# Kernel tuning notes

Measured on AMD Instinct MI355X. Metric: run time of the kernel, lower is better.

Reference implementation:

```python
import jax, jax.numpy as jnp
import numpy as np

B, T, C = 8, 2048, 768
HEAD = 64
NUM_REL = 2048


def setup_inputs() -> dict:
    key = jax.random.key(0)
    k1, k2, k3, k4, k5 = jax.random.split(key, 5)
    input_tensor = jax.random.normal(k1, (B, T, C), dtype=jnp.float32)
    # torch Linear(C, HEAD, bias=False): y = x @ W.T, W:[HEAD,C]; store as [C,HEAD]
    Wq = jax.random.normal(k2, (C, HEAD), dtype=jnp.float32) * (C ** -0.5)
    Wk = jax.random.normal(k3, (C, HEAD), dtype=jnp.float32) * (C ** -0.5)
    Wv = jax.random.normal(k4, (C, HEAD), dtype=jnp.float32) * (C ** -0.5)
    bias_table = jax.random.normal(k5, (NUM_REL, 1), dtype=jnp.float32)
    return {"input_tensor": input_tensor, "Wq": Wq, "Wk": Wk, "Wv": Wv, "bias_table": bias_table}


def reference(input_tensor, Wq, Wk, Wv, bias_table):
    Bsz, Tlen, _ = input_tensor.shape
    q = input_tensor @ Wq  # [B,T,H]
    k = input_tensor @ Wk
    v = input_tensor @ Wv
    scale = q.shape[-1] ** -0.5
    scores = jnp.einsum('bqh,bkh->bqk', q, k) * scale  # [B,T,T]
    # relative position bias: clamp(i - j, 0, NUM_REL-1)
    qpos = jnp.arange(Tlen)[:, None]
    kpos = jnp.arange(Tlen)[None, :]
    rel = jnp.clip(qpos - kpos, 0, bias_table.shape[0] - 1)
    bias = bias_table[rel, 0]  # [T,T]
    scores = scores + bias
    causal = kpos <= qpos  # True where allowed
    scores = jnp.where(causal, scores, -jnp.inf)
    attn = jax.nn.softmax(scores, axis=-1)
    return jnp.einsum('bqk,bkh->bqh', attn, v)
```

## Files before the change

kernel.cpp:

```cpp
#include <hip/hip_runtime.h>
#include <hip/hip_bf16.h>

typedef __attribute__((ext_vector_type(8))) short bf16x8;
typedef __attribute__((ext_vector_type(4))) short short4v;
typedef __attribute__((ext_vector_type(4))) float f32x4;

#define B_SZ 8
#define T_SZ 2048
#define C_SZ 768
#define H_SZ 64

__device__ __forceinline__ short f2bs(float f){
  __hip_bfloat16 h = __float2bfloat16(f);
  short s; __builtin_memcpy(&s, &h, 2); return s;
}
__device__ __forceinline__ f32x4 vmax4(f32x4 a, f32x4 b){
  f32x4 r; r[0]=fmaxf(a[0],b[0]); r[1]=fmaxf(a[1],b[1]);
  r[2]=fmaxf(a[2],b[2]); r[3]=fmaxf(a[3],b[3]); return r;
}
__device__ __forceinline__ void gload16(const void* g, void* l){
  __builtin_amdgcn_global_load_lds(
    (const __attribute__((address_space(1))) unsigned int*)g,
    (__attribute__((address_space(3))) unsigned int*)l, 16, 0, 0);
}

__global__ __launch_bounds__(256) void prep_wt(const float* __restrict__ Wq, const float* __restrict__ Wk,
                        const float* __restrict__ Wv, const float* __restrict__ bias,
                        short* __restrict__ Wt, float* __restrict__ bsc){
  int tid = threadIdx.x;
  if (blockIdx.x >= 36){
    int i = (blockIdx.x - 36)*256 + tid;
    bsc[i] = bias[i] * 1.44269504f;
    return;
  }
  __shared__ float tile[64][65];
  int mat = blockIdx.x / 12, kblk = blockIdx.x % 12;
  const float* W = (mat == 0) ? Wq : (mat == 1 ? Wk : Wv);
  int k0 = kblk * 64;
  int r = tid >> 2, cq = (tid & 3) * 16;
  #pragma unroll
  for (int i = 0; i < 4; ++i){
    float4 v = *reinterpret_cast<const float4*>(&W[(k0 + r)*H_SZ + cq + i*4]);
    tile[r][cq + i*4 + 0] = v.x; tile[r][cq + i*4 + 1] = v.y;
    tile[r][cq + i*4 + 2] = v.z; tile[r][cq + i*4 + 3] = v.w;
  }
  __syncthreads();
  int n = tid >> 2, kq = (tid & 3) * 16;
  bf16x8 o0, o1;
  #pragma unroll
  for (int e = 0; e < 8; ++e){
    o0[e] = f2bs(tile[kq + e][n]);
    o1[e] = f2bs(tile[kq + 8 + e][n]);
  }
  *reinterpret_cast<bf16x8*>(&Wt[(mat*64 + n)*C_SZ + k0 + kq])     = o0;
  *reinterpret_cast<bf16x8*>(&Wt[(mat*64 + n)*C_SZ + k0 + kq + 8]) = o1;
}

__global__ __launch_bounds__(512, 2) void qkv_gemm(const float* __restrict__ x, const short* __restrict__ Wt,
                         short* __restrict__ qb, short* __restrict__ kb, short* __restrict__ vT){
  __shared__ float As[2][2048];
  __shared__ short Bs[2][12288];
  int tid = threadIdx.x;
  int wv = tid >> 6, lane = tid & 63, lhi = lane >> 4, llo = lane & 15;
  int wm = wv >> 2, wn = wv & 3;
  long R0 = (long)blockIdx.x * 32;

  int srow = tid >> 4;
  int schunk = (tid & 15) ^ (srow & 7);
  const float* gsrcA = &x[(R0 + srow)*C_SZ + schunk*4];
  float* ldstA = &As[0][wv*256];

  int bn = tid >> 3;
  int bc = (tid & 7) ^ (bn & 7);
  const short* gsrcB0 = &Wt[(  0 + bn)*C_SZ + bc*8];
  const short* gsrcB1 = &Wt[( 64 + bn)*C_SZ + bc*8];
  const short* gsrcB2 = &Wt[(128 + bn)*C_SZ + bc*8];
  short* ldstB = &Bs[0][wv*512];

  f32x4 acc[3];
  #pragma unroll
  for (int j = 0; j < 3; ++j) acc[j] = (f32x4){0.f,0.f,0.f,0.f};

  int rr = wm*16 + llo;
  int r7 = rr & 7, lhi2 = lhi*2;
  int c0 = ((lhi2    ) ^ r7) << 2;
  int c1 = ((lhi2 + 1) ^ r7) << 2;
  int c2 = ((lhi2 + 8) ^ r7) << 2;
  int c3 = ((lhi2 + 9) ^ r7) << 2;
  int nrow[3];
  #pragma unroll
  for (int j = 0; j < 3; ++j) nrow[j] = (wn*48 + j*16 + llo)*64;
  int llo7 = llo & 7;
  int bo0 = ((    lhi) ^ llo7)*8;
  int bo1 = ((4 + lhi) ^ llo7)*8;

#define STAGE(T, BUF) { \
    gload16(gsrcA  + (T)*64, ldstA + (BUF)*2048); \
    gload16(gsrcB0 + (T)*64, ldstB + (BUF)*12288); \
    gload16(gsrcB1 + (T)*64, ldstB + (BUF)*12288 + 4096); \
    gload16(gsrcB2 + (T)*64, ldstB + (BUF)*12288 + 8192); }

  STAGE(0, 0);
  __syncthreads();

  for (int t = 0; t < 12; ++t){
    int cb = t & 1;
    if (t < 11) STAGE(t + 1, cb ^ 1);
    const float* Ar = &As[cb][rr*64];
    f32x4 a0 = *reinterpret_cast<const f32x4*>(Ar + c0);
    f32x4 a1 = *reinterpret_cast<const f32x4*>(Ar + c1);
    f32x4 a2 = *reinterpret_cast<const f32x4*>(Ar + c2);
    f32x4 a3 = *reinterpret_cast<const f32x4*>(Ar + c3);
    bf16x8 af0, af1;
    #pragma unroll
    for (int e = 0; e < 4; ++e){
      af0[e]   = f2bs(a0[e]); af0[4+e] = f2bs(a1[e]);
      af1[e]   = f2bs(a2[e]); af1[4+e] = f2bs(a3[e]);
    }
    const short* Br = &Bs[cb][0];
    #pragma unroll
    for (int j = 0; j < 3; ++j){
      bf16x8 b0 = *reinterpret_cast<const bf16x8*>(Br + nrow[j] + bo0);
      bf16x8 b1 = *reinterpret_cast<const bf16x8*>(Br + nrow[j] + bo1);
      acc[j] = __builtin_amdgcn_mfma_f32_16x16x32_bf16(af0, b0, acc[j], 0, 0, 0);
      acc[j] = __builtin_amdgcn_mfma_f32_16x16x32_bf16(af1, b1, acc[j], 0, 0, 0);
    }
    __syncthreads();
  }
#undef STAGE

  long mbase = R0 + wm*16 + lhi*4;
  #pragma unroll
  for (int j = 0; j < 3; ++j){
    int n = wn*48 + j*16 + llo;
    int mat = n >> 6, c = n & 63;
    if (mat == 2){
      long b = mbase >> 11, t = mbase & 2047;
      short4v p;
      #pragma unroll
      for (int reg = 0; reg < 4; ++reg) p[reg] = f2bs(acc[j][reg]);
      *reinterpret_cast<short4v*>(&vT[(b*H_SZ + c)*T_SZ + t]) = p;
    } else {
      short* dst = (mat == 0) ? qb : kb;
      #pragma unroll
      for (int reg = 0; reg < 4; ++reg)
        dst[(mbase + reg)*H_SZ + c] = f2bs(acc[j][reg]);
    }
  }
}

__global__ __launch_bounds__(512, 4) void attn_fwd(const short* __restrict__ qb, const short* __restrict__ kb,
                        const short* __restrict__ vT, const float* __restrict__ bsc,
                        float* __restrict__ out){
  __shared__ float bias_s[2048];
  __shared__ short P_lds[8][2][1152];
  __shared__ float m_part[8][16];
  __shared__ float l_part[8][4][16];
  float* OP = (float*)&P_lds[0][0][0];

  int tid = threadIdx.x;
  for (int i = tid; i < 2048; i += 512) bias_s[i] = bsc[i];

  int wv = tid >> 6, lane = tid & 63, lhi = lane >> 4, llo = lane & 15;
  int b = blockIdx.x & 7, jj = blockIdx.x >> 3;
  int qtA = jj, qtB = 127 - jj;
  int qA = qtA*16 + llo, qB = qtB*16 + llo;
  int nktA = (qtA >> 2) + 1, nktB = (qtB >> 2) + 1;

  const short* qrA = &qb[((long)(b*T_SZ + qA))*H_SZ + lhi*8];
  const short* qrB = &qb[((long)(b*T_SZ + qB))*H_SZ + lhi*8];
  bf16x8 qfA0 = *reinterpret_cast<const bf16x8*>(qrA);
  bf16x8 qfA1 = *reinterpret_cast<const bf16x8*>(qrA + 32);
  bf16x8 qfB0 = *reinterpret_cast<const bf16x8*>(qrB);
  bf16x8 qfB1 = *reinterpret_cast<const bf16x8*>(qrB + 32);
  const short* kbase = kb + (long)b*T_SZ*H_SZ;
  const short* vbase = vT + (long)b*H_SZ*T_SZ;
  __syncthreads();

  float mA = -1e30f, lA = 0.f, mB = -1e30f, lB = 0.f;
  f32x4 oA[4], oB[4];
  #pragma unroll
  for (int df = 0; df < 4; ++df){ oA[df] = (f32x4){0.f,0.f,0.f,0.f}; oB[df] = (f32x4){0.f,0.f,0.f,0.f}; }

#define SM(S, M, L, O, QV, TI, PB0, PB1) {                                  \
    _Pragma("unroll") for (int f = 0; f < 4; ++f)                           \
      _Pragma("unroll") for (int rg = 0; rg < 4; ++rg){                     \
        int kv = kv0 + f*16 + lhi*4 + rg;                                   \
        int rel = (QV) - kv;                                                \
        float bv = bias_s[rel > 0 ? rel : 0];                               \
        S[f][rg] = (rel >= 0) ? fmaf(S[f][rg], 0.18033688f, bv) : -1e30f; } \
    f32x4 tm = vmax4(vmax4(S[0], S[1]), vmax4(S[2], S[3]));                 \
    float pmax = fmaxf(fmaxf(tm[0], tm[1]), fmaxf(tm[2], tm[3]));           \
    if (!__all(pmax <= M + 8.0f)){                                          \
      float rm = fmaxf(pmax, __shfl_xor(pmax, 16));                         \
      rm = fmaxf(rm, __shfl_xor(rm, 32));                                   \
      float mnew = fmaxf(M, rm);                                            \
      float corr = exp2f(M - mnew);                                         \
      M = mnew; L *= corr;                                                  \
      _Pragma("unroll") for (int df = 0; df < 4; ++df) O[df] = O[df]*corr; }\
    _Pragma("unroll") for (int f = 0; f < 4; ++f){                          \
      short4v pk;                                                           \
      _Pragma("unroll") for (int rg = 0; rg < 4; ++rg){                     \
        float p = exp2f(S[f][rg] - M); S[f][rg] = p; pk[rg] = f2bs(p); }    \
      *reinterpret_cast<short4v*>(&P_lds[wv][TI][llo*72 + f*16 + lhi*4]) = pk; } \
    f32x4 va = (S[0] + S[1]) + (S[2] + S[3]);                               \
    L += (va[0] + va[1]) + (va[2] + va[3]);                                 \
    PB0 = *reinterpret_cast<const bf16x8*>(&P_lds[wv][TI][llo*72 + lhi*8]); \
    PB1 = *reinterpret_cast<const bf16x8*>(&P_lds[wv][TI][llo*72 + 32 + lhi*8]); }

  for (int c = wv; c < nktB; c += 8){
    int kv0 = c * 64;
    bool doA = c < nktA;
    f32x4 sA[4], sB[4];
    #pragma unroll
    for (int f = 0; f < 4; ++f){
      const short* kr = kbase + (long)(kv0 + f*16 + llo)*H_SZ + lhi*8;
      bf16x8 k0 = *reinterpret_cast<const bf16x8*>(kr);
      bf16x8 k1 = *reinterpret_cast<const bf16x8*>(kr + 32);
      f32x4 t = (f32x4){0.f,0.f,0.f,0.f};
      t = __builtin_amdgcn_mfma_f32_16x16x32_bf16(k0, qfB0, t, 0, 0, 0);
      t = __builtin_amdgcn_mfma_f32_16x16x32_bf16(k1, qfB1, t, 0, 0, 0);
      sB[f] = t;
      f32x4 u = (f32x4){0.f,0.f,0.f,0.f};
      u = __builtin_amdgcn_mfma_f32_16x16x32_bf16(k0, qfA0, u, 0, 0, 0);
      u = __builtin_amdgcn_mfma_f32_16x16x32_bf16(k1, qfA1, u, 0, 0, 0);
      sA[f] = u;
    }
    bf16x8 pbB0, pbB1;
    SM(sB, mB, lB, oB, qB, 1, pbB0, pbB1);
    if (doA){
      bf16x8 pbA0, pbA1;
      SM(sA, mA, lA, oA, qA, 0, pbA0, pbA1);
      #pragma unroll
      for (int df = 0; df < 4; ++df){
        const short* vr = vbase + (long)(df*16 + llo)*T_SZ + kv0 + lhi*8;
        bf16x8 v0 = *reinterpret_cast<const bf16x8*>(vr);
        bf16x8 v1 = *reinterpret_cast<const bf16x8*>(vr + 32);
        oB[df] = __builtin_amdgcn_mfma_f32_16x16x32_bf16(v0, pbB0, oB[df], 0, 0, 0);
        oB[df] = __builtin_amdgcn_mfma_f32_16x16x32_bf16(v1, pbB1, oB[df], 0, 0, 0);
        oA[df] = __builtin_amdgcn_mfma_f32_16x16x32_bf16(v0, pbA0, oA[df], 0, 0, 0);
        oA[df] = __builtin_amdgcn_mfma_f32_16x16x32_bf16(v1, pbA1, oA[df], 0, 0, 0);
      }
    } else {
      #pragma unroll
      for (int df = 0; df < 4; ++df){
        const short* vr = vbase + (long)(df*16 + llo)*T_SZ + kv0 + lhi*8;
        bf16x8 v0 = *reinterpret_cast<const bf16x8*>(vr);
        bf16x8 v1 = *reinterpret_cast<const bf16x8*>(vr + 32);
        oB[df] = __builtin_amdgcn_mfma_f32_16x16x32_bf16(v0, pbB0, oB[df], 0, 0, 0);
        oB[df] = __builtin_amdgcn_mfma_f32_16x16x32_bf16(v1, pbB1, oB[df], 0, 0, 0);
      }
    }
  }
#undef SM

#define MERGE(O, M, L, QT) {                                                \
    _Pragma("unroll") for (int df = 0; df < 4; ++df)                        \
      _Pragma("unroll") for (int rg = 0; rg < 4; ++rg)                      \
        OP[wv*1152 + llo*65 + df*16 + lhi*4 + rg] = O[df][rg];              \
    l_part[wv][lhi][llo] = L;                                               \
    if (lhi == 0) m_part[wv][llo] = M;                                      \
    __syncthreads();                                                        \
    { int idx = tid;                                                        \
      _Pragma("unroll") for (int rep = 0; rep < 2; ++rep){                  \
        int row = idx >> 6, d = idx & 63;                                   \
        float mstar = m_part[0][row];                                       \
        _Pragma("unroll") for (int w = 1; w < 8; ++w)                       \
          mstar = fmaxf(mstar, m_part[w][row]);                             \
        float lsum = 0.f, osum = 0.f;                                       \
        _Pragma("unroll") for (int w = 0; w < 8; ++w){                      \
          float sc = exp2f(m_part[w][row] - mstar);                         \
          lsum += sc * (l_part[w][0][row] + l_part[w][1][row]               \
                      + l_part[w][2][row] + l_part[w][3][row]);             \
          osum += sc * OP[w*1152 + row*65 + d]; }                           \
        out[((long)(b*T_SZ + (QT)*16 + row))*H_SZ + d] = osum / lsum;       \
        idx += 512; } }                                                     \
    __syncthreads(); }

  MERGE(oB, mB, lB, qtB);
  MERGE(oA, mA, lA, qtA);
#undef MERGE
}

extern "C" void kernel_launch(void* const* d_in, const int* in_sizes, int n_in,
                              void* d_out, int out_size, void* d_ws, size_t ws_size,
                              hipStream_t stream){
  const float* x    = (const float*)d_in[0];
  const float* Wq   = (const float*)d_in[1];
  const float* Wk   = (const float*)d_in[2];
  const float* Wv   = (const float*)d_in[3];
  const float* bias = (const float*)d_in[4];
  float* out = (float*)d_out;

  const size_t NTOK = (size_t)B_SZ * T_SZ * H_SZ;
  short* qb = (short*)d_ws;
  short* kb = qb + NTOK;
  short* vT = kb + NTOK;
  short* Wt = vT + NTOK;
  float* bsc = (float*)(Wt + 192*C_SZ);

  prep_wt<<<44, 256, 0, stream>>>(Wq, Wk, Wv, bias, Wt, bsc);
  qkv_gemm<<<512, 512, 0, stream>>>(x, Wt, qb, kb, vT);
  attn_fwd<<<512, 512, 0, stream>>>(qb, kb, vT, bsc, out);
}
```

Before: 58.33 us.

## Triple-buffer QKV GEMM with smaller K tiles and raise MFMA wave priority

```diff
diff --git a/kernel.cpp b/kernel.cpp
--- a/kernel.cpp
+++ b/kernel.cpp
@@ -58,74 +58,72 @@
 
 __global__ __launch_bounds__(512, 2) void qkv_gemm(const float* __restrict__ x, const short* __restrict__ Wt,
                          short* __restrict__ qb, short* __restrict__ kb, short* __restrict__ vT){
-  __shared__ float As[2][2048];
-  __shared__ short Bs[2][12288];
+  __shared__ float As[3][1024];
+  __shared__ short Bs[3][6144];
   int tid = threadIdx.x;
   int wv = tid >> 6, lane = tid & 63, lhi = lane >> 4, llo = lane & 15;
   int wm = wv >> 2, wn = wv & 3;
   long R0 = (long)blockIdx.x * 32;
 
-  int srow = tid >> 4;
-  int schunk = (tid & 15) ^ (srow & 7);
-  const float* gsrcA = &x[(R0 + srow)*C_SZ + schunk*4];
-  float* ldstA = &As[0][wv*256];
-
-  int bn = tid >> 3;
-  int bc = (tid & 7) ^ (bn & 7);
-  const short* gsrcB0 = &Wt[(  0 + bn)*C_SZ + bc*8];
-  const short* gsrcB1 = &Wt[( 64 + bn)*C_SZ + bc*8];
-  const short* gsrcB2 = &Wt[(128 + bn)*C_SZ + bc*8];
-  short* ldstB = &Bs[0][wv*512];
+  int r8 = lane >> 3, p8 = lane & 7;
+  int r4 = lane >> 2, p4 = lane & 3;
+  const char* src0; int sstr0; char* dst0; int dstr0;
+  if (wv < 4){
+    src0 = (const char*)&x[(R0 + wv*8 + r8)*C_SZ + ((p8 ^ (r8 & 7)) << 2)];
+    sstr0 = C_SZ ? 128 : 0;
+    sstr0 = 128;
+    dst0 = (char*)&As[0][wv*256]; dstr0 = 4096;
+  } else {
+    src0 = (const char*)&Wt[((wv-4)*16 + r4)*C_SZ + ((p4 ^ (r4 & 3)) << 3)];
+    sstr0 = 64;
+    dst0 = (char*)&Bs[0][(wv-4)*512]; dstr0 = 12288;
+  }
+  const char* src1 = (const char*)&Wt[((4+wv)*16 + r4)*C_SZ + ((p4 ^ (r4 & 3)) << 3)];
+  char* dst1 = (char*)&Bs[0][(4+wv)*512];
+
+#define STAGE(T, BUF) { \
+    gload16(src0 + (T)*sstr0, dst0 + (BUF)*dstr0); \
+    gload16(src1 + (T)*64,    dst1 + (BUF)*12288); }
 
   f32x4 acc[3];
   #pragma unroll
   for (int j = 0; j < 3; ++j) acc[j] = (f32x4){0.f,0.f,0.f,0.f};
 
   int rr = wm*16 + llo;
-  int r7 = rr & 7, lhi2 = lhi*2;
-  int c0 = ((lhi2    ) ^ r7) << 2;
-  int c1 = ((lhi2 + 1) ^ r7) << 2;
-  int c2 = ((lhi2 + 8) ^ r7) << 2;
-  int c3 = ((lhi2 + 9) ^ r7) << 2;
-  int nrow[3];
-  #pragma unroll
-  for (int j = 0; j < 3; ++j) nrow[j] = (wn*48 + j*16 + llo)*64;
-  int llo7 = llo & 7;
-  int bo0 = ((    lhi) ^ llo7)*8;
-  int bo1 = ((4 + lhi) ^ llo7)*8;
-
-#define STAGE(T, BUF) { \
-    gload16(gsrcA  + (T)*64, ldstA + (BUF)*2048); \
-    gload16(gsrcB0 + (T)*64, ldstB + (BUF)*12288); \
-    gload16(gsrcB1 + (T)*64, ldstB + (BUF)*12288 + 4096); \
-    gload16(gsrcB2 + (T)*64, ldstB + (BUF)*12288 + 8192); }
+  int r7 = rr & 7;
+  int c0x = rr*32 + (((2*lhi    ) ^ r7) << 2);
+  int c1x = rr*32 + (((2*lhi + 1) ^ r7) << 2);
+  int nof[3];
+  #pragma unroll
+  for (int j = 0; j < 3; ++j){
+    int n = wn*48 + j*16 + llo;
+    nof[j] = n*32 + ((lhi ^ (n & 3)) << 3);
+  }
 
   STAGE(0, 0);
-  __syncthreads();
-
-  for (int t = 0; t < 12; ++t){
-    int cb = t & 1;
-    if (t < 11) STAGE(t + 1, cb ^ 1);
-    const float* Ar = &As[cb][rr*64];
-    f32x4 a0 = *reinterpret_cast<const f32x4*>(Ar + c0);
-    f32x4 a1 = *reinterpret_cast<const f32x4*>(Ar + c1);
-    f32x4 a2 = *reinterpret_cast<const f32x4*>(Ar + c2);
-    f32x4 a3 = *reinterpret_cast<const f32x4*>(Ar + c3);
-    bf16x8 af0, af1;
+  STAGE(1, 1);
+
+  #pragma unroll
+  for (int t = 0; t < 24; ++t){
+    if (t < 23) asm volatile("s_waitcnt vmcnt(2)" ::: "memory");
+    else        asm volatile("s_waitcnt vmcnt(0)" ::: "memory");
+    __builtin_amdgcn_sched_barrier(0);
+    __builtin_amdgcn_s_barrier();
+    __builtin_amdgcn_sched_barrier(0);
+    if (t < 22) STAGE(t + 2, (t + 2) % 3);
+    int cb = t % 3;
+    const float* Ar = &As[cb][0];
+    f32x4 a0 = *reinterpret_cast<const f32x4*>(Ar + c0x);
+    f32x4 a1 = *reinterpret_cast<const f32x4*>(Ar + c1x);
+    bf16x8 af;
     #pragma unroll
-    for (int e = 0; e < 4; ++e){
-      af0[e]   = f2bs(a0[e]); af0[4+e] = f2bs(a1[e]);
-      af1[e]   = f2bs(a2[e]); af1[4+e] = f2bs(a3[e]);
-    }
+    for (int e = 0; e < 4; ++e){ af[e] = f2bs(a0[e]); af[4+e] = f2bs(a1[e]); }
     const short* Br = &Bs[cb][0];
     #pragma unroll
     for (int j = 0; j < 3; ++j){
-      bf16x8 b0 = *reinterpret_cast<const bf16x8*>(Br + nrow[j] + bo0);
-      bf16x8 b1 = *reinterpret_cast<const bf16x8*>(Br + nrow[j] + bo1);
-      acc[j] = __builtin_amdgcn_mfma_f32_16x16x32_bf16(af0, b0, acc[j], 0, 0, 0);
-      acc[j] = __builtin_amdgcn_mfma_f32_16x16x32_bf16(af1, b1, acc[j], 0, 0, 0);
+      bf16x8 bf = *reinterpret_cast<const bf16x8*>(Br + nof[j]);
+      acc[j] = __builtin_amdgcn_mfma_f32_16x16x32_bf16(af, bf, acc[j], 0, 0, 0);
     }
-    __syncthreads();
   }
 #undef STAGE
 
@@ -212,6 +210,7 @@
     int kv0 = c * 64;
     bool doA = c < nktA;
     f32x4 sA[4], sB[4];
+    __builtin_amdgcn_s_setprio(1);
     #pragma unroll
     for (int f = 0; f < 4; ++f){
       const short* kr = kbase + (long)(kv0 + f*16 + llo)*H_SZ + lhi*8;
@@ -226,11 +225,13 @@
       u = __builtin_amdgcn_mfma_f32_16x16x32_bf16(k1, qfA1, u, 0, 0, 0);
       sA[f] = u;
     }
+    __builtin_amdgcn_s_setprio(0);
     bf16x8 pbB0, pbB1;
     SM(sB, mB, lB, oB, qB, 1, pbB0, pbB1);
     if (doA){
       bf16x8 pbA0, pbA1;
       SM(sA, mA, lA, oA, qA, 0, pbA0, pbA1);
+      __builtin_amdgcn_s_setprio(1);
       #pragma unroll
       for (int df = 0; df < 4; ++df){
         const short* vr = vbase + (long)(df*16 + llo)*T_SZ + kv0 + lhi*8;
@@ -241,7 +242,9 @@
         oA[df] = __builtin_amdgcn_mfma_f32_16x16x32_bf16(v0, pbA0, oA[df], 0, 0, 0);
         oA[df] = __builtin_amdgcn_mfma_f32_16x16x32_bf16(v1, pbA1, oA[df], 0, 0, 0);
       }
+      __builtin_amdgcn_s_setprio(0);
     } else {
+      __builtin_amdgcn_s_setprio(1);
       #pragma unroll
       for (int df = 0; df < 4; ++df){
         const short* vr = vbase + (long)(df*16 + llo)*T_SZ + kv0 + lhi*8;
@@ -250,6 +253,7 @@
         oB[df] = __builtin_amdgcn_mfma_f32_16x16x32_bf16(v0, pbB0, oB[df], 0, 0, 0);
         oB[df] = __builtin_amdgcn_mfma_f32_16x16x32_bf16(v1, pbB1, oB[df], 0, 0, 0);
       }
+      __builtin_amdgcn_s_setprio(0);
     }
   }
 #undef SM
```

Result: slower. 62.11 us (+6.5%).
